# Optimization experiments

Measured on AMD Instinct MI355X. Metric: run time of the kernel, lower is better.

The kernel has to match this reference:

```python
import jax, jax.numpy as jnp
import numpy as np

N_USERS = 50000
N_ITEMS = 50000
N_NODES = N_USERS + N_ITEMS
N_EDGES = 1600000
D_IN = 128
D_OUT = 128


def setup_inputs() -> dict:
    key = jax.random.key(0)
    k1, k2, k3, k4, k5, k6 = jax.random.split(key, 6)
    u_f = jax.random.normal(k1, (N_USERS, D_IN), dtype=jnp.float32)
    v_f = jax.random.normal(k2, (N_ITEMS, D_IN), dtype=jnp.float32)
    adj_rows = jax.random.randint(k3, (N_EDGES,), 0, N_NODES, dtype=jnp.int32)
    adj_cols = jax.random.randint(k4, (N_EDGES,), 0, N_NODES, dtype=jnp.int32)
    adj_vals = jax.random.uniform(k5, (N_EDGES,), dtype=jnp.float32)
    # xavier_uniform init for weight [in_feats, out_feats]
    bound = float(np.sqrt(6.0 / (D_IN + D_OUT)))
    weight = jax.random.uniform(k6, (D_IN, D_OUT), dtype=jnp.float32,
                                minval=-bound, maxval=bound)
    return {"u_f": u_f, "v_f": v_f, "adj_rows": adj_rows,
            "adj_cols": adj_cols, "adj_vals": adj_vals, "weight": weight}


def reference(u_f, v_f, adj_rows, adj_cols, adj_vals, weight):
    # node_f = cat([u_f, v_f]) @ W          -- dense transform
    node_f = jnp.concatenate([u_f, v_f], axis=0)          # [N, D_in]
    node_f = node_f @ weight                               # [N, D_out]
    # sparse adjacency matmul: out[r] = sum_e vals[e] * node_f[cols[e]]
    msgs = adj_vals[:, None] * node_f[adj_cols]            # [E, D_out]
    out = jax.ops.segment_sum(msgs, adj_rows, num_segments=N_NODES)
    # activation (relu)
    return jax.nn.relu(out)
```

## Files before the change

kernel.cpp:

```cpp
#include <hip/hip_runtime.h>
#include <hip/hip_bf16.h>
#include <hip/hip_fp16.h>

#define N_USERS 50000
#define N_NODES 100000
#define N_EDGES 1600000
#define DIM 128
#define CAP 64

#define RPB 128
#define NBINS ((N_NODES + RPB - 1) / RPB)
#define BINCAP 4096
#define EPB 8192
#define FILL_BLOCKS ((N_EDGES + EPB - 1) / EPB)
#define GEMM_BLOCKS 1024
#define WFRAG_ELEMS (32 * 64 * 8)

typedef __attribute__((ext_vector_type(8))) _Float16 half8;
typedef __attribute__((ext_vector_type(4))) _Float16 half4;
typedef __attribute__((ext_vector_type(4))) float f32x4;

__global__ void prep_kernel(const float* __restrict__ W,
                            _Float16* __restrict__ wfrag_g,
                            int* __restrict__ gcount) {
    if (blockIdx.x == 64) {
        for (int b = threadIdx.x; b < NBINS; b += 256) gcount[b] = 0;
        return;
    }
    const int f   = blockIdx.x * 256 + threadIdx.x;
    const int ts  = f >> 9;
    const int rem = f & 511;
    const int ln  = rem >> 3;
    const int j   = rem & 7;
    const int t   = ts >> 2;
    const int s   = ts & 3;
    const int krow = s * 32 + (ln >> 4) * 8 + j;
    const int col  = t * 16 + (ln & 15);
    wfrag_g[f] = (_Float16)W[krow * DIM + col];
}

__device__ __forceinline__ void gemm_main(
        const float* __restrict__ u_f, const float* __restrict__ v_f,
        _Float16* __restrict__ node_f, const _Float16* wfrag,
        int blockId, int nBlocks) {
    const int tid  = threadIdx.x;
    const int lane = tid & 63;
    const int wave = tid >> 6;
    const int m    = lane & 15;
    const int quad = lane >> 4;
    const int n_wtiles = N_NODES / 16;

    for (int wt = blockId * 4 + wave; wt < n_wtiles; wt += nBlocks * 4) {
        const int row = wt * 16 + m;
        const float* src = (row < N_USERS) ? u_f + (size_t)row * DIM
                                           : v_f + (size_t)(row - N_USERS) * DIM;
        f32x4 acc[8];
        #pragma unroll
        for (int t = 0; t < 8; ++t) acc[t] = (f32x4){0.f, 0.f, 0.f, 0.f};

        #pragma unroll
        for (int s = 0; s < 4; ++s) {
            const float* ap = src + s * 32 + quad * 8;
            const float4 a0 = *(const float4*)ap;
            const float4 a1 = *(const float4*)(ap + 4);
            half8 af;
            af[0] = (_Float16)a0.x; af[1] = (_Float16)a0.y;
            af[2] = (_Float16)a0.z; af[3] = (_Float16)a0.w;
            af[4] = (_Float16)a1.x; af[5] = (_Float16)a1.y;
            af[6] = (_Float16)a1.z; af[7] = (_Float16)a1.w;
            #pragma unroll
            for (int t = 0; t < 8; ++t) {
                const half8 wf = *(const half8*)&wfrag[((t * 4 + s) * 64 + lane) * 8];
                acc[t] = __builtin_amdgcn_mfma_f32_16x16x32_f16(af, wf, acc[t], 0, 0, 0);
            }
        }

        const int base = wt * 16;
        #pragma unroll
        for (int t = 0; t < 8; ++t) {
            #pragma unroll
            for (int r = 0; r < 4; ++r) {
                const int orow = base + quad * 4 + r;
                node_f[(size_t)orow * DIM + t * 16 + m] = (_Float16)acc[t][r];
            }
        }
    }
}

__global__ __launch_bounds__(256) void gemm_kernel(
        const float* __restrict__ u_f, const float* __restrict__ v_f,
        const _Float16* __restrict__ wfrag_g, _Float16* __restrict__ node_f) {
    __shared__ _Float16 wfrag[WFRAG_ELEMS];
    const int4* src = (const int4*)wfrag_g;
    int4* dst = (int4*)wfrag;
    #pragma unroll
    for (int i = 0; i < WFRAG_ELEMS / 8 / 256; ++i)
        dst[i * 256 + threadIdx.x] = src[i * 256 + threadIdx.x];
    __syncthreads();
    gemm_main(u_f, v_f, node_f, wfrag, blockIdx.x, GEMM_BLOCKS);
}

__global__ __launch_bounds__(256) void fill_kernel(
        const int* __restrict__ rows, const int* __restrict__ cols,
        const float* __restrict__ vals,
        int* __restrict__ gcount, long long* __restrict__ bin_data) {
    __shared__ int hist[NBINS];
    __shared__ int base_[NBINS];

    const int bb  = blockIdx.x;
    const int tid = threadIdx.x;
    const int e0  = bb * EPB;

    for (int b = tid; b < NBINS; b += 256) hist[b] = 0;
    __syncthreads();

    unsigned meta[EPB / 256];
    #pragma unroll
    for (int i = 0; i < EPB / 256; ++i) {
        const int e = e0 + i * 256 + tid;
        if (e < N_EDGES) {
            const int row = rows[e];
            const int bin = row >> 7;
            const int pos = atomicAdd(&hist[bin], 1);
            meta[i] = ((unsigned)bin << 20) | ((unsigned)(row & 127) << 13)
                    | (unsigned)pos;
        } else {
            meta[i] = 0xFFFFFFFFu;
        }
    }
    __syncthreads();

    for (int b = tid; b < NBINS; b += 256) {
        const int h = hist[b];
        base_[b] = h ? atomicAdd(&gcount[b], h) : 0;
    }
    __syncthreads();

    #pragma unroll
    for (int i = 0; i < EPB / 256; ++i) {
        if (meta[i] == 0xFFFFFFFFu) continue;
        const int e   = e0 + i * 256 + tid;
        const int bin = meta[i] >> 20;
        const int rl  = (meta[i] >> 13) & 127;
        const int pos = meta[i] & 0x1FFF;
        const int idx = base_[bin] + pos;
        if (idx < BINCAP) {
            const unsigned w0 = ((unsigned)rl << 17) | (unsigned)cols[e];
            const long long ent =
                ((long long)__float_as_int(vals[e]) << 32) | (long long)w0;
            bin_data[(size_t)bin * BINCAP + idx] = ent;
        }
    }
}

__global__ __launch_bounds__(256) void gemm_mfma_kernel(
        const float* __restrict__ u_f, const float* __restrict__ v_f,
        const float* __restrict__ W, _Float16* __restrict__ node_f) {
    __shared__ _Float16 wfrag[WFRAG_ELEMS];
    const int tid = threadIdx.x;
    for (int f = tid * 64, end = tid * 64 + 64; f < end; ++f) {
        const int ts   = f >> 9;
        const int rem  = f & 511;
        const int ln   = rem >> 3;
        const int j    = rem & 7;
        const int t    = ts >> 2;
        const int s    = ts & 3;
        const int krow = s * 32 + (ln >> 4) * 8 + j;
        const int col  = t * 16 + (ln & 15);
        wfrag[f] = (_Float16)W[krow * DIM + col];
    }
    __syncthreads();
    gemm_main(u_f, v_f, node_f, wfrag, blockIdx.x, gridDim.x);
}

__global__ __launch_bounds__(1024) void bin_gather_kernel(
        const _Float16* __restrict__ node_f, const int* __restrict__ gcount,
        const long long* __restrict__ bin_data, float* __restrict__ out) {
    __shared__ unsigned list[RPB][CAP];
    __shared__ int rowcnt[RPB];

    const int bin  = blockIdx.x;
    const int tid  = threadIdx.x;
    const int row0 = bin * RPB;
    const int nrows = (N_NODES - row0 < RPB) ? (N_NODES - row0) : RPB;

    if (tid < RPB) rowcnt[tid] = 0;
    __syncthreads();

    int n = gcount[bin];
    if (n > BINCAP) n = BINCAP;
    for (int k = tid; k < n; k += 1024) {
        const long long ent = bin_data[(size_t)bin * BINCAP + k];
        const unsigned w0 = (unsigned)ent;
        const float v = __int_as_float((int)(ent >> 32));
        const int rl = (int)(w0 >> 17);
        const int pos = atomicAdd(&rowcnt[rl], 1);
        if (pos < CAP) {
            const int q = (int)(v * 32767.f + 0.5f);
            list[rl][pos] = ((unsigned)q << 17) | (w0 & 0x1FFFFu);
        }
    }
    __syncthreads();

    const int wave = tid >> 6;
    const int lane = tid & 63;
    const int pid  = lane >> 4;
    const int cl   = lane & 15;

    for (int rp = 0; rp < 8; ++rp) {
        const int rl = rp * 16 + wave;
        if (rl >= nrows) break;
        const int row = row0 + rl;

        int cnt = rowcnt[rl];
        if (cnt > CAP) cnt = CAP;

        int   col = 0;
        float val = 0.f;
        if (lane < cnt) {
            const unsigned p = list[rl][lane];
            col = (int)(p & 0x1FFFFu);
            val = (float)(p >> 17) * (1.f / 32767.f);
        }

        float acc[8];
        #pragma unroll
        for (int i = 0; i < 8; ++i) acc[i] = 0.f;

        int j = 0;
        for (; j + 16 <= cnt; j += 16) {
            int c[4]; float v[4]; half8 h[4];
            #pragma unroll
            for (int q = 0; q < 4; ++q) {
                c[q] = __shfl(col, j + 4 * q + pid, 64);
                v[q] = __shfl(val, j + 4 * q + pid, 64);
            }
            #pragma unroll
            for (int q = 0; q < 4; ++q)
                h[q] = *(const half8*)&node_f[(size_t)c[q] * DIM + cl * 8];
            #pragma unroll
            for (int q = 0; q < 4; ++q) {
                #pragma unroll
                for (int i = 0; i < 8; ++i)
                    acc[i] += v[q] * (float)h[q][i];
            }
        }
        for (; j + 4 <= cnt; j += 4) {
            const int   c = __shfl(col, j + pid, 64);
            const float v = __shfl(val, j + pid, 64);
            const half8 h = *(const half8*)&node_f[(size_t)c * DIM + cl * 8];
            #pragma unroll
            for (int i = 0; i < 8; ++i)
                acc[i] += v * (float)h[i];
        }
        if (j < cnt) {
            const int rem = cnt - j;
            const int sj  = j + (pid < rem ? pid : 0);
            const int   c = __shfl(col, sj, 64);
            const float v = __shfl(val, sj, 64);
            if (pid < rem) {
                const half8 h = *(const half8*)&node_f[(size_t)c * DIM + cl * 8];
                #pragma unroll
                for (int i = 0; i < 8; ++i)
                    acc[i] += v * (float)h[i];
            }
        }

        #pragma unroll
        for (int i = 0; i < 8; ++i) {
            acc[i] += __shfl_xor(acc[i], 16, 64);
            acc[i] += __shfl_xor(acc[i], 32, 64);
        }

        if (pid == 0) {
            f32x4 r0, r1;
            #pragma unroll
            for (int i = 0; i < 4; ++i) {
                r0[i] = acc[i]     > 0.f ? acc[i]     : 0.f;
                r1[i] = acc[i + 4] > 0.f ? acc[i + 4] : 0.f;
            }
            float* dst = &out[(size_t)row * DIM + cl * 8];
            __builtin_nontemporal_store(r0, (f32x4*)dst);
            __builtin_nontemporal_store(r1, (f32x4*)(dst + 4));
        }
    }
}

__global__ void zero_out_kernel(float* __restrict__ out) {
    int i = blockIdx.x * blockDim.x + threadIdx.x;
    int idx = i * 4;
    if (idx < N_NODES * DIM) {
        float4 z = {0.f, 0.f, 0.f, 0.f};
        *(float4*)&out[idx] = z;
    }
}

__global__ void scatter_kernel(const _Float16* __restrict__ node_f,
                               const int* __restrict__ rows, const int* __restrict__ cols,
                               const float* __restrict__ vals, float* __restrict__ out) {
    int t = blockIdx.x * blockDim.x + threadIdx.x;
    int e = t >> 5;
    int part = t & 31;
    if (e >= N_EDGES) return;
    int r = rows[e], c = cols[e];
    float v = vals[e];
    const __half2 h0 = *(const __half2*)&node_f[(size_t)c * DIM + part * 4];
    const __half2 h1 = *(const __half2*)&node_f[(size_t)c * DIM + part * 4 + 2];
    const float2 f0 = __half22float2(h0);
    const float2 f1 = __half22float2(h1);
    float* dst = &out[(size_t)r * DIM + part * 4];
    unsafeAtomicAdd(dst + 0, v * f0.x);
    unsafeAtomicAdd(dst + 1, v * f0.y);
    unsafeAtomicAdd(dst + 2, v * f1.x);
    unsafeAtomicAdd(dst + 3, v * f1.y);
}

__global__ void relu_kernel(float* __restrict__ out) {
    int i = blockIdx.x * blockDim.x + threadIdx.x;
    int idx = i * 4;
    if (idx < N_NODES * DIM) {
        float4 v = *(float4*)&out[idx];
        v.x = v.x > 0.f ? v.x : 0.f;
        v.y = v.y > 0.f ? v.y : 0.f;
        v.z = v.z > 0.f ? v.z : 0.f;
        v.w = v.w > 0.f ? v.w : 0.f;
        *(float4*)&out[idx] = v;
    }
}

extern "C" void kernel_launch(void* const* d_in, const int* in_sizes, int n_in,
                              void* d_out, int out_size, void* d_ws, size_t ws_size,
                              hipStream_t stream) {
    const float* u_f  = (const float*)d_in[0];
    const float* v_f  = (const float*)d_in[1];
    const int*   rows = (const int*)d_in[2];
    const int*   cols = (const int*)d_in[3];
    const float* vals = (const float*)d_in[4];
    const float* W    = (const float*)d_in[5];
    float* out = (float*)d_out;

    char* ws = (char*)d_ws;
    const size_t nodef_bytes   = (size_t)N_NODES * DIM * 2;
    const size_t gcount_bytes  = 4096;
    const size_t bindata_bytes = (size_t)NBINS * BINCAP * 8;
    const size_t wfrag_bytes   = (size_t)WFRAG_ELEMS * 2;

    _Float16* node_f = (_Float16*)ws;
    int* gcount = (int*)(ws + nodef_bytes);
    long long* bin_data = (long long*)(ws + nodef_bytes + gcount_bytes);
    _Float16* wfrag_g = (_Float16*)(ws + nodef_bytes + gcount_bytes + bindata_bytes);

    if (ws_size >= nodef_bytes + gcount_bytes + bindata_bytes + wfrag_bytes) {
        prep_kernel<<<65, 256, 0, stream>>>(W, wfrag_g, gcount);
        gemm_kernel<<<GEMM_BLOCKS, 256, 0, stream>>>(u_f, v_f, wfrag_g, node_f);
        fill_kernel<<<FILL_BLOCKS, 256, 0, stream>>>(rows, cols, vals, gcount, bin_data);
        bin_gather_kernel<<<NBINS, 1024, 0, stream>>>(
            node_f, gcount, bin_data, out);
    } else {
        gemm_mfma_kernel<<<512, 256, 0, stream>>>(u_f, v_f, W, node_f);
        zero_out_kernel<<<(N_NODES * DIM / 4 + 255) / 256, 256, 0, stream>>>(out);
        scatter_kernel<<<((size_t)N_EDGES * 32 + 255) / 256, 256, 0, stream>>>(
            node_f, rows, cols, vals, out);
        relu_kernel<<<(N_NODES * DIM / 4 + 255) / 256, 256, 0, stream>>>(out);
    }
}
```

Measured before the change: 244.0 us.

## Fuse GEMM and edge binning into one launch; halve gather block size

Merges the dense GEMM kernel and the edge bin-fill kernel into a single grid, where the first blocks run the GEMM and the remaining blocks do the histogram/bin scatter, sharing LDS through a union. This removes one launch and lets the two independent phases run concurrently on the GPU. Separately, the gather kernel drops from 1024 to 512 threads per block, with each wave handling twice as many rows, to allow more resident blocks. The risk is LDS union sizing lowering occupancy for fill blocks, and fewer threads for the bin-list staging phase.

```diff
diff --git a/kernel.cpp b/kernel.cpp
--- a/kernel.cpp
+++ b/kernel.cpp
@@ -14,6 +14,7 @@
 #define EPB 8192
 #define FILL_BLOCKS ((N_EDGES + EPB - 1) / EPB)
 #define GEMM_BLOCKS 1024
+#define FUSED_GRID (GEMM_BLOCKS + FILL_BLOCKS)
 #define WFRAG_ELEMS (32 * 64 * 8)
 
 typedef __attribute__((ext_vector_type(8))) _Float16 half8;
@@ -87,31 +88,33 @@
     }
 }
 
-__global__ __launch_bounds__(256) void gemm_kernel(
+__global__ __launch_bounds__(256) void fused_gemm_fill_kernel(
         const float* __restrict__ u_f, const float* __restrict__ v_f,
-        const _Float16* __restrict__ wfrag_g, _Float16* __restrict__ node_f) {
-    __shared__ _Float16 wfrag[WFRAG_ELEMS];
-    const int4* src = (const int4*)wfrag_g;
-    int4* dst = (int4*)wfrag;
-    #pragma unroll
-    for (int i = 0; i < WFRAG_ELEMS / 8 / 256; ++i)
-        dst[i * 256 + threadIdx.x] = src[i * 256 + threadIdx.x];
-    __syncthreads();
-    gemm_main(u_f, v_f, node_f, wfrag, blockIdx.x, GEMM_BLOCKS);
-}
-
-__global__ __launch_bounds__(256) void fill_kernel(
+        const _Float16* __restrict__ wfrag_g, _Float16* __restrict__ node_f,
         const int* __restrict__ rows, const int* __restrict__ cols,
         const float* __restrict__ vals,
         int* __restrict__ gcount, long long* __restrict__ bin_data) {
-    __shared__ int hist[NBINS];
-    __shared__ int base_[NBINS];
-
-    const int bb  = blockIdx.x;
+    __shared__ union {
+        _Float16 wfrag[WFRAG_ELEMS];
+        struct { int hist[NBINS]; int base_[NBINS]; } a;
+    } sh;
+
+    if (blockIdx.x < GEMM_BLOCKS) {
+        const int4* src = (const int4*)wfrag_g;
+        int4* dst = (int4*)sh.wfrag;
+        #pragma unroll
+        for (int i = 0; i < WFRAG_ELEMS / 8 / 256; ++i)
+            dst[i * 256 + threadIdx.x] = src[i * 256 + threadIdx.x];
+        __syncthreads();
+        gemm_main(u_f, v_f, node_f, sh.wfrag, blockIdx.x, GEMM_BLOCKS);
+        return;
+    }
+
+    const int bb  = blockIdx.x - GEMM_BLOCKS;
     const int tid = threadIdx.x;
     const int e0  = bb * EPB;
 
-    for (int b = tid; b < NBINS; b += 256) hist[b] = 0;
+    for (int b = tid; b < NBINS; b += 256) sh.a.hist[b] = 0;
     __syncthreads();
 
     unsigned meta[EPB / 256];
@@ -121,7 +124,7 @@
         if (e < N_EDGES) {
             const int row = rows[e];
             const int bin = row >> 7;
-            const int pos = atomicAdd(&hist[bin], 1);
+            const int pos = atomicAdd(&sh.a.hist[bin], 1);
             meta[i] = ((unsigned)bin << 20) | ((unsigned)(row & 127) << 13)
                     | (unsigned)pos;
         } else {
@@ -131,8 +134,8 @@
     __syncthreads();
 
     for (int b = tid; b < NBINS; b += 256) {
-        const int h = hist[b];
-        base_[b] = h ? atomicAdd(&gcount[b], h) : 0;
+        const int h = sh.a.hist[b];
+        sh.a.base_[b] = h ? atomicAdd(&gcount[b], h) : 0;
     }
     __syncthreads();
 
@@ -143,7 +146,7 @@
         const int bin = meta[i] >> 20;
         const int rl  = (meta[i] >> 13) & 127;
         const int pos = meta[i] & 0x1FFF;
-        const int idx = base_[bin] + pos;
+        const int idx = sh.a.base_[bin] + pos;
         if (idx < BINCAP) {
             const unsigned w0 = ((unsigned)rl << 17) | (unsigned)cols[e];
             const long long ent =
@@ -173,7 +176,7 @@
     gemm_main(u_f, v_f, node_f, wfrag, blockIdx.x, gridDim.x);
 }
 
-__global__ __launch_bounds__(1024) void bin_gather_kernel(
+__global__ __launch_bounds__(512) void bin_gather_kernel(
         const _Float16* __restrict__ node_f, const int* __restrict__ gcount,
         const long long* __restrict__ bin_data, float* __restrict__ out) {
     __shared__ unsigned list[RPB][CAP];
@@ -189,7 +192,7 @@
 
     int n = gcount[bin];
     if (n > BINCAP) n = BINCAP;
-    for (int k = tid; k < n; k += 1024) {
+    for (int k = tid; k < n; k += 512) {
         const long long ent = bin_data[(size_t)bin * BINCAP + k];
         const unsigned w0 = (unsigned)ent;
         const float v = __int_as_float((int)(ent >> 32));
@@ -207,8 +210,8 @@
     const int pid  = lane >> 4;
     const int cl   = lane & 15;
 
-    for (int rp = 0; rp < 8; ++rp) {
-        const int rl = rp * 16 + wave;
+    for (int rp = 0; rp < 16; ++rp) {
+        const int rl = rp * 8 + wave;
         if (rl >= nrows) break;
         const int row = row0 + rl;
 
@@ -352,9 +355,9 @@
 
     if (ws_size >= nodef_bytes + gcount_bytes + bindata_bytes + wfrag_bytes) {
         prep_kernel<<<65, 256, 0, stream>>>(W, wfrag_g, gcount);
-        gemm_kernel<<<GEMM_BLOCKS, 256, 0, stream>>>(u_f, v_f, wfrag_g, node_f);
-        fill_kernel<<<FILL_BLOCKS, 256, 0, stream>>>(rows, cols, vals, gcount, bin_data);
-        bin_gather_kernel<<<NBINS, 1024, 0, stream>>>(
+        fused_gemm_fill_kernel<<<FUSED_GRID, 256, 0, stream>>>(
+            u_f, v_f, wfrag_g, node_f, rows, cols, vals, gcount, bin_data);
+        bin_gather_kernel<<<NBINS, 512, 0, stream>>>(
             node_f, gcount, bin_data, out);
     } else {
         gemm_mfma_kernel<<<512, 256, 0, stream>>>(u_f, v_f, W, node_f);
```

New measurement: 255.3 us. 1.05x slower.
